# Kernel tuning notes

Hardware: AMD Instinct MI355X
Metric: run time of the kernel (lower is better)

Reference implementation:

```python
import jax, jax.numpy as jnp
import numpy as np

B, N, D, E, S, H = 4, 1024, 1024, 32, 1, 4096
LN_EPS = 1e-5
PSIM_EPS = 1e-9


def _layernorm(x, g, b):
    m = x.mean(axis=-1, keepdims=True)
    v = ((x - m) ** 2).mean(axis=-1, keepdims=True)
    return (x - m) * jax.lax.rsqrt(v + LN_EPS) * g + b


def setup_inputs() -> dict:
    key = jax.random.key(0)
    ks = jax.random.split(key, 4)
    x = jax.random.normal(ks[0], (B, N, D), jnp.float32)
    phi = jax.random.normal(ks[1], (E, S, D), jnp.float32) / np.float32(np.sqrt(D))
    w1 = jax.random.normal(ks[2], (E, D, H), jnp.float32) / np.float32(np.sqrt(D))
    w2 = jax.random.normal(ks[3], (E, H, D), jnp.float32) / np.float32(np.sqrt(H))
    return {
        "x": x,
        "phi": phi,
        "key_gamma": jnp.ones((D,), jnp.float32),
        "key_beta": jnp.zeros((D,), jnp.float32),
        "query_gamma": jnp.ones((D,), jnp.float32),
        "query_beta": jnp.zeros((D,), jnp.float32),
        "ln_gamma": jnp.ones((D,), jnp.float32),
        "ln_beta": jnp.zeros((D,), jnp.float32),
        "scale": jnp.float32(1.0),
        "w1": w1,
        "b1": jnp.zeros((E, H), jnp.float32),
        "w2": w2,
        "b2": jnp.zeros((E, D), jnp.float32),
    }


def _forward(x, phi, key_gamma, key_beta, query_gamma, query_beta,
             ln_gamma, ln_beta, scale, w1, b1, w2, b2):
    # key = OffsetScale(x); norm is Identity (slot_layernorm=True)
    k = x * key_gamma + key_beta                       # [B,N,D]
    # query = LayerNorm(OffsetScale(phi)) * scale
    q = _layernorm(phi * query_gamma + query_beta, ln_gamma, ln_beta) * scale  # [E,S,D]
    logits = jnp.einsum('bnd,esd->bnes', k, q)         # [B,N,E,S]
    dispatch_weights = jax.nn.softmax(logits, axis=1)  # softmax over tokens N
    combine_weights = jax.nn.softmax(logits.reshape(B, N, E * S), axis=-1)  # over slots
    slots = jnp.einsum('bnd,bnes->besd', x, dispatch_weights)  # [B,E,S,D]
    # per-expert 2-layer GELU MLP (MultiExpertLayer)
    h = jax.nn.gelu(jnp.einsum('besd,edh->besh', slots, w1) + b1[None, :, None, :], approximate=False)
    expert_out = jnp.einsum('besh,ehd->besd', h, w2) + b2[None, :, None, :]
    out = jnp.einsum('besd,bnes->bnd',
                     expert_out,
                     combine_weights.reshape(B, N, E, S))  # [B,N,D]
    return out, dispatch_weights, combine_weights.reshape(B, N, E, S)


def _metrics(combine_weights, dispatch_weights):
    # combine similarity: normalize over (E,S), flatten, per-(B,N) outer product
    cw = combine_weights  # [B,N,E,S]
    cn = cw * jax.lax.rsqrt((cw ** 2).sum(axis=(2, 3), keepdims=True) + PSIM_EPS)
    cf = cn.reshape(B, N, E * S)
    cw_sim = jnp.einsum('bni,bnj->bnij', cf, cf)       # [B,N,ES,ES]
    cw_metric = (cw_sim.sum() - jnp.diagonal(cw_sim, axis1=1, axis2=2).sum()) / (B * N * (N - 1))
    # dispatch similarity: permute to [B,E,S,N], normalize over N
    dp = dispatch_weights.transpose(0, 2, 3, 1)        # [B,E,S,N]
    dn = dp * jax.lax.rsqrt((dp ** 2).sum(axis=-1, keepdims=True) + PSIM_EPS)
    dw_sim = jnp.einsum('besi,besj->besij', dn, dn)    # [B,E,S,N,N]
    dw_metric = (dw_sim.sum() - jnp.diagonal(dw_sim, axis1=1, axis2=2).sum()) / (B * E * S * (E * S - 1))
    return cw_metric, dw_metric


def reference(x, phi, key_gamma, key_beta, query_gamma, query_beta,
              ln_gamma, ln_beta, scale, w1, b1, w2, b2):
    out, dispatch_weights, combine_weights = _forward(
        x, phi, key_gamma, key_beta, query_gamma, query_beta,
        ln_gamma, ln_beta, scale, w1, b1, w2, b2)
    cw_metric, dw_metric = _metrics(combine_weights, dispatch_weights)
    return out, cw_metric, dw_metric
```

## Files before the change

### kernel.cpp

```cpp
#include <hip/hip_runtime.h>
#include <math.h>

#define BB 4
#define NN 1024
#define DD 1024
#define EE 32
#define HH 4096

#define Q_OFF      0
#define LOGITS_OFF 32768
#define DWT_OFF    163840
#define CW_OFF     294912
#define SLOTS_OFF  425984
#define HBUF_OFF   557056
#define GBUF_OFF   1081344
#define EO_OFF     1605632
#define MACC_OFF   1736704
#define WS_TOTAL   1736708

__global__ __launch_bounds__(256) void q_kernel(
    const float* __restrict__ phi, const float* __restrict__ qg,
    const float* __restrict__ qb, const float* __restrict__ lng,
    const float* __restrict__ lnb, const float* __restrict__ scale,
    float* __restrict__ q)
{
    int e = blockIdx.x, t = threadIdx.x;
    float v[4]; float s = 0.f, s2 = 0.f;
    #pragma unroll
    for (int i = 0; i < 4; ++i) {
        int d = i*256 + t;
        float xv = phi[e*DD + d]*qg[d] + qb[d];
        v[i] = xv; s += xv; s2 += xv*xv;
    }
    #pragma unroll
    for (int o = 32; o > 0; o >>= 1) { s += __shfl_xor(s, o); s2 += __shfl_xor(s2, o); }
    __shared__ float ra[4], rb[4];
    if ((t & 63) == 0) { ra[t>>6] = s; rb[t>>6] = s2; }
    __syncthreads();
    s  = ra[0]+ra[1]+ra[2]+ra[3];
    s2 = rb[0]+rb[1]+rb[2]+rb[3];
    float mean = s * (1.f/DD);
    float var  = s2 * (1.f/DD) - mean*mean;
    float r = rsqrtf(var + 1e-5f);
    float sc = scale[0];
    #pragma unroll
    for (int i = 0; i < 4; ++i) {
        int d = i*256 + t;
        q[e*DD + d] = ((v[i]-mean)*r*lng[d] + lnb[d]) * sc;
    }
}

__global__ __launch_bounds__(256) void logits_kernel(
    const float* __restrict__ x, const float* __restrict__ kg,
    const float* __restrict__ kb, const float* __restrict__ q,
    float* __restrict__ logits)
{
    int w = threadIdx.x >> 6, l = threadIdx.x & 63;
    int row = blockIdx.x*4 + w;
    const float* xr = x + (size_t)row * DD;
    float acc[EE];
    #pragma unroll
    for (int e = 0; e < EE; ++e) acc[e] = 0.f;
    #pragma unroll
    for (int i = 0; i < 4; ++i) {
        int d0 = i*256 + l*4;
        float4 xv = *(const float4*)(xr + d0);
        float4 g  = *(const float4*)(kg + d0);
        float4 bv = *(const float4*)(kb + d0);
        float4 kv;
        kv.x = xv.x*g.x + bv.x; kv.y = xv.y*g.y + bv.y;
        kv.z = xv.z*g.z + bv.z; kv.w = xv.w*g.w + bv.w;
        #pragma unroll
        for (int e = 0; e < EE; ++e) {
            float4 qv = *(const float4*)(q + e*DD + d0);
            acc[e] += kv.x*qv.x + kv.y*qv.y + kv.z*qv.z + kv.w*qv.w;
        }
    }
    #pragma unroll
    for (int e = 0; e < EE; ++e) {
        float a = acc[e];
        #pragma unroll
        for (int o = 32; o > 0; o >>= 1) a += __shfl_xor(a, o);
        if (l == 0) logits[(size_t)row*EE + e] = a;
    }
}

__global__ __launch_bounds__(256) void dsoftmax_kernel(
    const float* __restrict__ logits, float* __restrict__ dwT,
    float* __restrict__ macc)
{
    int be = blockIdx.x; int b = be >> 5, e = be & 31;
    int t = threadIdx.x;
    __shared__ float red[4];
    const float* lb = logits + (size_t)b*NN*EE + e;
    float v[4]; float m = -1e30f;
    #pragma unroll
    for (int i = 0; i < 4; ++i) {
        v[i] = lb[(size_t)(i*256 + t)*EE];
        m = fmaxf(m, v[i]);
    }
    #pragma unroll
    for (int o = 32; o > 0; o >>= 1) m = fmaxf(m, __shfl_xor(m, o));
    if ((t & 63) == 0) red[t>>6] = m;
    __syncthreads();
    m = fmaxf(fmaxf(red[0], red[1]), fmaxf(red[2], red[3]));
    __syncthreads();
    float p[4]; float z = 0.f;
    #pragma unroll
    for (int i = 0; i < 4; ++i) { p[i] = expf(v[i]-m); z += p[i]; }
    #pragma unroll
    for (int o = 32; o > 0; o >>= 1) z += __shfl_xor(z, o);
    if ((t & 63) == 0) red[t>>6] = z;
    __syncthreads();
    z = red[0]+red[1]+red[2]+red[3];
    __syncthreads();
    float rz = 1.f / z;
    float s2 = 0.f;
    float* dp = dwT + ((size_t)b*EE + e)*NN;
    #pragma unroll
    for (int i = 0; i < 4; ++i) {
        float pv = p[i]*rz;
        dp[i*256+t] = pv;
        s2 += pv*pv;
    }
    #pragma unroll
    for (int o = 32; o > 0; o >>= 1) s2 += __shfl_xor(s2, o);
    if ((t & 63) == 0) red[t>>6] = s2;
    __syncthreads();
    if (t == 0) {
        float tot = red[0]+red[1]+red[2]+red[3];
        float rd2 = 1.f / (tot + 1e-9f);
        atomicAdd(&macc[2], rd2);
        if (e == 0) atomicAdd(&macc[3], rd2);
    }
}

__global__ __launch_bounds__(256) void csoftmax_kernel(
    const float* __restrict__ logits, float* __restrict__ cw,
    float* __restrict__ macc)
{
    int t = threadIdx.x, sub = t >> 5, e = t & 31;
    int row = blockIdx.x*8 + sub;
    float v = logits[(size_t)row*EE + e];
    float m = v;
    #pragma unroll
    for (int o = 16; o > 0; o >>= 1) m = fmaxf(m, __shfl_xor(m, o));
    float p = expf(v - m);
    float z = p;
    #pragma unroll
    for (int o = 16; o > 0; o >>= 1) z += __shfl_xor(z, o);
    p = p / z;
    cw[(size_t)row*EE + e] = p;
    float s2 = p*p, s1 = p;
    #pragma unroll
    for (int o = 16; o > 0; o >>= 1) { s2 += __shfl_xor(s2, o); s1 += __shfl_xor(s1, o); }
    float r = rsqrtf(s2 + 1e-9f);
    float cf = p*r, R = s1*r;
    __shared__ float rr[8];
    if (e == 0) rr[sub] = R*R;
    __syncthreads();
    if (t == 0) atomicAdd(&macc[0], rr[0]+rr[1]+rr[2]+rr[3]+rr[4]+rr[5]+rr[6]+rr[7]);
    int n = row & (NN-1);
    if (n < EE && e == n) atomicAdd(&macc[1], cf*R);
}

__global__ __launch_bounds__(256) void slots_kernel(
    const float* __restrict__ x, const float* __restrict__ dwT,
    float* __restrict__ slots)
{
    int nt = blockIdx.x;
    int e0 = blockIdx.y * 16;
    int b  = blockIdx.z;
    int t = threadIdx.x;
    __shared__ float wv[16][32];
    for (int i = t; i < 512; i += 256) {
        int e = i >> 5, n = i & 31;
        wv[e][n] = dwT[((size_t)b*EE + e0 + e)*NN + nt*32 + n];
    }
    __syncthreads();
    float4 acc[16];
    #pragma unroll
    for (int e = 0; e < 16; ++e) acc[e] = make_float4(0.f,0.f,0.f,0.f);
    const float* xb = x + (size_t)b*NN*DD + (size_t)(nt*32)*DD + t*4;
    for (int n = 0; n < 32; ++n) {
        float4 xv = *(const float4*)(xb + (size_t)n*DD);
        #pragma unroll
        for (int e = 0; e < 16; ++e) {
            float wgt = wv[e][n];
            acc[e].x += wgt*xv.x; acc[e].y += wgt*xv.y;
            acc[e].z += wgt*xv.z; acc[e].w += wgt*xv.w;
        }
    }
    #pragma unroll
    for (int e = 0; e < 16; ++e) {
        float* sp = slots + ((size_t)b*EE + e0 + e)*DD + t*4;
        atomicAdd(sp+0, acc[e].x); atomicAdd(sp+1, acc[e].y);
        atomicAdd(sp+2, acc[e].z); atomicAdd(sp+3, acc[e].w);
    }
}

__global__ __launch_bounds__(256) void w1_kernel(
    const float* __restrict__ slots, const float* __restrict__ w1,
    float* __restrict__ hbuf)
{
    int kt = blockIdx.x;
    int ht = blockIdx.y;
    int e  = blockIdx.z;
    int t = threadIdx.x;
    __shared__ __align__(16) float sT[512][4];
    for (int i = t; i < 2048; i += 256) {
        int b = i >> 9, d = i & 511;
        sT[d][b] = slots[((size_t)b*EE + e)*DD + kt*512 + d];
    }
    __syncthreads();
    int h0 = ht*1024 + t*4;
    float4 a0 = make_float4(0.f,0.f,0.f,0.f), a1 = a0, a2 = a0, a3 = a0;
    const float* wp = w1 + ((size_t)e*DD + kt*512)*HH + h0;
    #pragma unroll 4
    for (int d = 0; d < 512; ++d) {
        float4 w = *(const float4*)(wp + (size_t)d*HH);
        float4 s = *(const float4*)(&sT[d][0]);
        a0.x += s.x*w.x; a0.y += s.x*w.y; a0.z += s.x*w.z; a0.w += s.x*w.w;
        a1.x += s.y*w.x; a1.y += s.y*w.y; a1.z += s.y*w.z; a1.w += s.y*w.w;
        a2.x += s.z*w.x; a2.y += s.z*w.y; a2.z += s.z*w.z; a2.w += s.z*w.w;
        a3.x += s.w*w.x; a3.y += s.w*w.y; a3.z += s.w*w.z; a3.w += s.w*w.w;
    }
    float* hp = hbuf + (size_t)e*4*HH + h0;
    atomicAdd(hp+0,      a0.x); atomicAdd(hp+1,      a0.y); atomicAdd(hp+2,      a0.z); atomicAdd(hp+3,      a0.w);
    atomicAdd(hp+HH+0,   a1.x); atomicAdd(hp+HH+1,   a1.y); atomicAdd(hp+HH+2,   a1.z); atomicAdd(hp+HH+3,   a1.w);
    atomicAdd(hp+2*HH+0, a2.x); atomicAdd(hp+2*HH+1, a2.y); atomicAdd(hp+2*HH+2, a2.z); atomicAdd(hp+2*HH+3, a2.w);
    atomicAdd(hp+3*HH+0, a3.x); atomicAdd(hp+3*HH+1, a3.y); atomicAdd(hp+3*HH+2, a3.z); atomicAdd(hp+3*HH+3, a3.w);
}

__global__ __launch_bounds__(256) void gelu_kernel(
    const float* __restrict__ hbuf, const float* __restrict__ b1,
    float* __restrict__ gbuf)
{
    int idx = blockIdx.x*256 + threadIdx.x;
    #pragma unroll
    for (int i = 0; i < 4; ++i) {
        int j = idx + i*131072;
        int e = j >> 14, h = j & (HH-1);
        float v = hbuf[j] + b1[(e << 12) + h];
        gbuf[j] = 0.5f * v * (1.f + erff(v * 0.70710678118654752f));
    }
}

__global__ __launch_bounds__(256) void w2_kernel(
    const float* __restrict__ gbuf, const float* __restrict__ w2,
    float* __restrict__ eo)
{
    int kt = blockIdx.x;
    int e  = blockIdx.y;
    int t = threadIdx.x;
    __shared__ __align__(16) float gT[256][4];
    for (int i = t; i < 1024; i += 256) {
        int b = i >> 8, h = i & 255;
        gT[h][b] = gbuf[((size_t)e*4 + b)*HH + kt*256 + h];
    }
    __syncthreads();
    int d0 = t*4;
    float4 a0 = make_float4(0.f,0.f,0.f,0.f), a1 = a0, a2 = a0, a3 = a0;
    const float* wp = w2 + ((size_t)e*HH + kt*256)*DD + d0;
    #pragma unroll 4
    for (int h = 0; h < 256; ++h) {
        float4 w = *(const float4*)(wp + (size_t)h*DD);
        float4 g = *(const float4*)(&gT[h][0]);
        a0.x += g.x*w.x; a0.y += g.x*w.y; a0.z += g.x*w.z; a0.w += g.x*w.w;
        a1.x += g.y*w.x; a1.y += g.y*w.y; a1.z += g.y*w.z; a1.w += g.y*w.w;
        a2.x += g.z*w.x; a2.y += g.z*w.y; a2.z += g.z*w.z; a2.w += g.z*w.w;
        a3.x += g.w*w.x; a3.y += g.w*w.y; a3.z += g.w*w.z; a3.w += g.w*w.w;
    }
    #pragma unroll
    for (int b = 0; b < 4; ++b) {
        float4 a = (b==0)?a0:(b==1)?a1:(b==2)?a2:a3;
        float* ep = eo + ((size_t)b*EE + e)*DD + d0;
        atomicAdd(ep+0, a.x); atomicAdd(ep+1, a.y);
        atomicAdd(ep+2, a.z); atomicAdd(ep+3, a.w);
    }
}

__global__ __launch_bounds__(256) void b2_kernel(float* __restrict__ eo, const float* __restrict__ b2)
{
    int idx = blockIdx.x*256 + threadIdx.x;
    #pragma unroll
    for (int i = 0; i < 4; ++i) {
        int j = idx + i*32768;
        eo[j] += b2[j & 32767];
    }
}

__global__ __launch_bounds__(256) void combine_kernel(
    const float* __restrict__ cw, const float* __restrict__ eo,
    float* __restrict__ out)
{
    int nt = blockIdx.x;
    int b  = blockIdx.y;
    int t = threadIdx.x;
    __shared__ __align__(16) float cwl[16][32];
    for (int i = t; i < 512; i += 256) {
        int r = i >> 5, e = i & 31;
        cwl[r][e] = cw[((size_t)b*NN + nt*16 + r)*EE + e];
    }
    __syncthreads();
    float4 acc[16];
    #pragma unroll
    for (int r = 0; r < 16; ++r) acc[r] = make_float4(0.f,0.f,0.f,0.f);
    const float* ep = eo + (size_t)b*EE*DD + t*4;
    #pragma unroll
    for (int e4 = 0; e4 < 8; ++e4) {
        float4 w0 = *(const float4*)(ep + (size_t)(e4*4+0)*DD);
        float4 w1v = *(const float4*)(ep + (size_t)(e4*4+1)*DD);
        float4 w2v = *(const float4*)(ep + (size_t)(e4*4+2)*DD);
        float4 w3v = *(const float4*)(ep + (size_t)(e4*4+3)*DD);
        #pragma unroll
        for (int r = 0; r < 16; ++r) {
            float4 c = *(const float4*)(&cwl[r][e4*4]);
            acc[r].x += c.x*w0.x + c.y*w1v.x + c.z*w2v.x + c.w*w3v.x;
            acc[r].y += c.x*w0.y + c.y*w1v.y + c.z*w2v.y + c.w*w3v.y;
            acc[r].z += c.x*w0.z + c.y*w1v.z + c.z*w2v.z + c.w*w3v.z;
            acc[r].w += c.x*w0.w + c.y*w1v.w + c.z*w2v.w + c.w*w3v.w;
        }
    }
    #pragma unroll
    for (int r = 0; r < 16; ++r) {
        *(float4*)(out + ((size_t)b*NN + nt*16 + r)*DD + t*4) = acc[r];
    }
}

__global__ void finalize_kernel(const float* __restrict__ macc, float* __restrict__ out)
{
    out[4194304] = (macc[0] - macc[1]) * (1.f / 4190208.f);
    out[4194305] = (macc[2] - macc[3]) * (1.f / 3968.f);
}

extern "C" void kernel_launch(void* const* d_in, const int* in_sizes, int n_in,
                              void* d_out, int out_size, void* d_ws, size_t ws_size,
                              hipStream_t stream) {
    const float* x   = (const float*)d_in[0];
    const float* phi = (const float*)d_in[1];
    const float* kg  = (const float*)d_in[2];
    const float* kb  = (const float*)d_in[3];
    const float* qg  = (const float*)d_in[4];
    const float* qb  = (const float*)d_in[5];
    const float* lng = (const float*)d_in[6];
    const float* lnb = (const float*)d_in[7];
    const float* sc  = (const float*)d_in[8];
    const float* w1  = (const float*)d_in[9];
    const float* b1  = (const float*)d_in[10];
    const float* w2  = (const float*)d_in[11];
    const float* b2  = (const float*)d_in[12];
    float* out = (float*)d_out;
    float* ws  = (float*)d_ws;

    float* q      = ws + Q_OFF;
    float* logits = ws + LOGITS_OFF;
    float* dwT    = ws + DWT_OFF;
    float* cw     = ws + CW_OFF;
    float* slots  = ws + SLOTS_OFF;
    float* hbuf   = ws + HBUF_OFF;
    float* gbuf   = ws + GBUF_OFF;
    float* eo     = ws + EO_OFF;
    float* macc   = ws + MACC_OFF;

    hipMemsetAsync(ws + SLOTS_OFF, 0, (size_t)(WS_TOTAL - SLOTS_OFF)*sizeof(float), stream);

    q_kernel<<<32, 256, 0, stream>>>(phi, qg, qb, lng, lnb, sc, q);
    logits_kernel<<<1024, 256, 0, stream>>>(x, kg, kb, q, logits);
    dsoftmax_kernel<<<128, 256, 0, stream>>>(logits, dwT, macc);
    csoftmax_kernel<<<512, 256, 0, stream>>>(logits, cw, macc);
    slots_kernel<<<dim3(32,2,4), 256, 0, stream>>>(x, dwT, slots);
    w1_kernel<<<dim3(2,4,32), 256, 0, stream>>>(slots, w1, hbuf);
    gelu_kernel<<<512, 256, 0, stream>>>(hbuf, b1, gbuf);
    w2_kernel<<<dim3(16,32), 256, 0, stream>>>(gbuf, w2, eo);
    b2_kernel<<<128, 256, 0, stream>>>(eo, b2);
    combine_kernel<<<dim3(64,4), 256, 0, stream>>>(cw, eo, out);
    finalize_kernel<<<1, 1, 0, stream>>>(macc, out);
}
```

Before: 1.181 ms.

## Replace atomic split-K accumulation with partial buffers and fused reductions

The float atomicAdd accumulation in the slots, w1 and w2 kernels is replaced by plain float4 stores into per-split partial buffers, which are then reduced deterministically. The GELU step is folded into the w2 kernel's smem load, which also sums the w1 partials and adds b1, and the b2 bias add is folded into a new partial-reduction kernel. The w1 split-K is doubled to 4 chunks for more blocks and unroll is raised. The large workspace memset shrinks to just the metric accumulators. The cost is extra partial-buffer traffic (around 36 MB of writes and reads) and one extra reduction launch.

```diff
diff --git a/kernel.cpp b/kernel.cpp
--- a/kernel.cpp
+++ b/kernel.cpp
@@ -12,11 +12,12 @@
 #define DWT_OFF    163840
 #define CW_OFF     294912
 #define SLOTS_OFF  425984
-#define HBUF_OFF   557056
-#define GBUF_OFF   1081344
-#define EO_OFF     1605632
-#define MACC_OFF   1736704
-#define WS_TOTAL   1736708
+#define SPART_OFF  557056
+#define HPART_OFF  4751360
+#define EPART_OFF  6848512
+#define EO_OFF     8945664
+#define MACC_OFF   9076736
+#define WS_TOTAL   9076740
 
 __global__ __launch_bounds__(256) void q_kernel(
     const float* __restrict__ phi, const float* __restrict__ qg,
@@ -166,7 +167,7 @@
 
 __global__ __launch_bounds__(256) void slots_kernel(
     const float* __restrict__ x, const float* __restrict__ dwT,
-    float* __restrict__ slots)
+    float* __restrict__ spart)
 {
     int nt = blockIdx.x;
     int e0 = blockIdx.y * 16;
@@ -193,31 +194,42 @@
     }
     #pragma unroll
     for (int e = 0; e < 16; ++e) {
-        float* sp = slots + ((size_t)b*EE + e0 + e)*DD + t*4;
-        atomicAdd(sp+0, acc[e].x); atomicAdd(sp+1, acc[e].y);
-        atomicAdd(sp+2, acc[e].z); atomicAdd(sp+3, acc[e].w);
-    }
+        *(float4*)(spart + (((size_t)nt*BB + b)*EE + e0 + e)*DD + t*4) = acc[e];
+    }
+}
+
+__global__ __launch_bounds__(256) void sreduce_kernel(
+    const float* __restrict__ spart, float* __restrict__ slots)
+{
+    int j = (blockIdx.x*256 + threadIdx.x)*4;
+    float4 a = make_float4(0.f,0.f,0.f,0.f);
+    #pragma unroll
+    for (int nt = 0; nt < 32; ++nt) {
+        float4 v = *(const float4*)(spart + (size_t)nt*(BB*EE*DD) + j);
+        a.x += v.x; a.y += v.y; a.z += v.z; a.w += v.w;
+    }
+    *(float4*)(slots + j) = a;
 }
 
 __global__ __launch_bounds__(256) void w1_kernel(
     const float* __restrict__ slots, const float* __restrict__ w1,
-    float* __restrict__ hbuf)
+    float* __restrict__ hpart)
 {
     int kt = blockIdx.x;
     int ht = blockIdx.y;
     int e  = blockIdx.z;
     int t = threadIdx.x;
-    __shared__ __align__(16) float sT[512][4];
-    for (int i = t; i < 2048; i += 256) {
-        int b = i >> 9, d = i & 511;
-        sT[d][b] = slots[((size_t)b*EE + e)*DD + kt*512 + d];
+    __shared__ __align__(16) float sT[256][4];
+    for (int i = t; i < 1024; i += 256) {
+        int b = i >> 8, d = i & 255;
+        sT[d][b] = slots[((size_t)b*EE + e)*DD + kt*256 + d];
     }
     __syncthreads();
     int h0 = ht*1024 + t*4;
     float4 a0 = make_float4(0.f,0.f,0.f,0.f), a1 = a0, a2 = a0, a3 = a0;
-    const float* wp = w1 + ((size_t)e*DD + kt*512)*HH + h0;
-    #pragma unroll 4
-    for (int d = 0; d < 512; ++d) {
+    const float* wp = w1 + ((size_t)e*DD + kt*256)*HH + h0;
+    #pragma unroll 8
+    for (int d = 0; d < 256; ++d) {
         float4 w = *(const float4*)(wp + (size_t)d*HH);
         float4 s = *(const float4*)(&sT[d][0]);
         a0.x += s.x*w.x; a0.y += s.x*w.y; a0.z += s.x*w.z; a0.w += s.x*w.w;
@@ -225,30 +237,16 @@
         a2.x += s.z*w.x; a2.y += s.z*w.y; a2.z += s.z*w.z; a2.w += s.z*w.w;
         a3.x += s.w*w.x; a3.y += s.w*w.y; a3.z += s.w*w.z; a3.w += s.w*w.w;
     }
-    float* hp = hbuf + (size_t)e*4*HH + h0;
-    atomicAdd(hp+0,      a0.x); atomicAdd(hp+1,      a0.y); atomicAdd(hp+2,      a0.z); atomicAdd(hp+3,      a0.w);
-    atomicAdd(hp+HH+0,   a1.x); atomicAdd(hp+HH+1,   a1.y); atomicAdd(hp+HH+2,   a1.z); atomicAdd(hp+HH+3,   a1.w);
-    atomicAdd(hp+2*HH+0, a2.x); atomicAdd(hp+2*HH+1, a2.y); atomicAdd(hp+2*HH+2, a2.z); atomicAdd(hp+2*HH+3, a2.w);
-    atomicAdd(hp+3*HH+0, a3.x); atomicAdd(hp+3*HH+1, a3.y); atomicAdd(hp+3*HH+2, a3.z); atomicAdd(hp+3*HH+3, a3.w);
-}
-
-__global__ __launch_bounds__(256) void gelu_kernel(
-    const float* __restrict__ hbuf, const float* __restrict__ b1,
-    float* __restrict__ gbuf)
-{
-    int idx = blockIdx.x*256 + threadIdx.x;
-    #pragma unroll
-    for (int i = 0; i < 4; ++i) {
-        int j = idx + i*131072;
-        int e = j >> 14, h = j & (HH-1);
-        float v = hbuf[j] + b1[(e << 12) + h];
-        gbuf[j] = 0.5f * v * (1.f + erff(v * 0.70710678118654752f));
-    }
+    float* hp = hpart + (((size_t)kt*EE + e)*BB)*HH + h0;
+    *(float4*)(hp)        = a0;
+    *(float4*)(hp + HH)   = a1;
+    *(float4*)(hp + 2*HH) = a2;
+    *(float4*)(hp + 3*HH) = a3;
 }
 
 __global__ __launch_bounds__(256) void w2_kernel(
-    const float* __restrict__ gbuf, const float* __restrict__ w2,
-    float* __restrict__ eo)
+    const float* __restrict__ hpart, const float* __restrict__ b1,
+    const float* __restrict__ w2, float* __restrict__ epart)
 {
     int kt = blockIdx.x;
     int e  = blockIdx.y;
@@ -256,13 +254,18 @@
     __shared__ __align__(16) float gT[256][4];
     for (int i = t; i < 1024; i += 256) {
         int b = i >> 8, h = i & 255;
-        gT[h][b] = gbuf[((size_t)e*4 + b)*HH + kt*256 + h];
+        int habs = kt*256 + h;
+        float v = b1[(size_t)e*HH + habs];
+        #pragma unroll
+        for (int k = 0; k < 4; ++k)
+            v += hpart[(((size_t)k*EE + e)*BB + b)*HH + habs];
+        gT[h][b] = 0.5f * v * (1.f + erff(v * 0.70710678118654752f));
     }
     __syncthreads();
     int d0 = t*4;
     float4 a0 = make_float4(0.f,0.f,0.f,0.f), a1 = a0, a2 = a0, a3 = a0;
     const float* wp = w2 + ((size_t)e*HH + kt*256)*DD + d0;
-    #pragma unroll 4
+    #pragma unroll 8
     for (int h = 0; h < 256; ++h) {
         float4 w = *(const float4*)(wp + (size_t)h*DD);
         float4 g = *(const float4*)(&gT[h][0]);
@@ -274,20 +277,22 @@
     #pragma unroll
     for (int b = 0; b < 4; ++b) {
         float4 a = (b==0)?a0:(b==1)?a1:(b==2)?a2:a3;
-        float* ep = eo + ((size_t)b*EE + e)*DD + d0;
-        atomicAdd(ep+0, a.x); atomicAdd(ep+1, a.y);
-        atomicAdd(ep+2, a.z); atomicAdd(ep+3, a.w);
-    }
-}
-
-__global__ __launch_bounds__(256) void b2_kernel(float* __restrict__ eo, const float* __restrict__ b2)
-{
-    int idx = blockIdx.x*256 + threadIdx.x;
-    #pragma unroll
-    for (int i = 0; i < 4; ++i) {
-        int j = idx + i*32768;
-        eo[j] += b2[j & 32767];
-    }
+        *(float4*)(epart + (((size_t)kt*BB + b)*EE + e)*DD + d0) = a;
+    }
+}
+
+__global__ __launch_bounds__(256) void b2red_kernel(
+    const float* __restrict__ epart, const float* __restrict__ b2,
+    float* __restrict__ eo)
+{
+    int j = (blockIdx.x*256 + threadIdx.x)*4;
+    float4 a = *(const float4*)(b2 + (j & 32767));
+    #pragma unroll
+    for (int kt = 0; kt < 16; ++kt) {
+        float4 v = *(const float4*)(epart + (size_t)kt*(BB*EE*DD) + j);
+        a.x += v.x; a.y += v.y; a.z += v.z; a.w += v.w;
+    }
+    *(float4*)(eo + j) = a;
 }
 
 __global__ __launch_bounds__(256) void combine_kernel(
@@ -358,22 +363,23 @@
     float* dwT    = ws + DWT_OFF;
     float* cw     = ws + CW_OFF;
     float* slots  = ws + SLOTS_OFF;
-    float* hbuf   = ws + HBUF_OFF;
-    float* gbuf   = ws + GBUF_OFF;
+    float* spart  = ws + SPART_OFF;
+    float* hpart  = ws + HPART_OFF;
+    float* epart  = ws + EPART_OFF;
     float* eo     = ws + EO_OFF;
     float* macc   = ws + MACC_OFF;
 
-    hipMemsetAsync(ws + SLOTS_OFF, 0, (size_t)(WS_TOTAL - SLOTS_OFF)*sizeof(float), stream);
+    hipMemsetAsync(macc, 0, 4*sizeof(float), stream);
 
     q_kernel<<<32, 256, 0, stream>>>(phi, qg, qb, lng, lnb, sc, q);
     logits_kernel<<<1024, 256, 0, stream>>>(x, kg, kb, q, logits);
     dsoftmax_kernel<<<128, 256, 0, stream>>>(logits, dwT, macc);
     csoftmax_kernel<<<512, 256, 0, stream>>>(logits, cw, macc);
-    slots_kernel<<<dim3(32,2,4), 256, 0, stream>>>(x, dwT, slots);
-    w1_kernel<<<dim3(2,4,32), 256, 0, stream>>>(slots, w1, hbuf);
-    gelu_kernel<<<512, 256, 0, stream>>>(hbuf, b1, gbuf);
-    w2_kernel<<<dim3(16,32), 256, 0, stream>>>(gbuf, w2, eo);
-    b2_kernel<<<128, 256, 0, stream>>>(eo, b2);
+    slots_kernel<<<dim3(32,2,4), 256, 0, stream>>>(x, dwT, spart);
+    sreduce_kernel<<<128, 256, 0, stream>>>(spart, slots);
+    w1_kernel<<<dim3(4,4,32), 256, 0, stream>>>(slots, w1, hpart);
+    w2_kernel<<<dim3(16,32), 256, 0, stream>>>(hpart, b1, w2, epart);
+    b2red_kernel<<<128, 256, 0, stream>>>(epart, b2, eo);
     combine_kernel<<<dim3(64,4), 256, 0, stream>>>(cw, eo, out);
     finalize_kernel<<<1, 1, 0, stream>>>(macc, out);
 }
```

New measurement: 1.103 ms. 6.6% less time.
